# Kernel optimization log

Measured on AMD Instinct MI355X. Metric: run time of the kernel, lower is better.

The kernel has to match this reference:

```python
import jax, jax.numpy as jnp
import numpy as np

M, N, T = 4, 48, 512
D_IN = M + N                 # GRU-net input dim (m+n)
H1 = D_IN * 10 * 8           # 4160
HID = M * M + N * N          # 2320 GRU hidden
H2 = M * N * 4               # 768
D_OUT = M * N                # 192


def setup_inputs() -> dict:
    key = jax.random.key(0)
    ks = jax.random.split(key, 12)
    s = lambda i, shape, sc=0.02: (jax.random.normal(ks[i], shape, jnp.float32) * sc)
    return {
        "A": jnp.eye(M, dtype=jnp.float32) + s(0, (M, M), 0.05),
        "C": s(1, (N, M + 1), 0.1),
        "x0": jax.random.normal(ks[2], (M,), jnp.float32),
        "h0": jax.random.normal(ks[3], (HID,), jnp.float32),  # randn init hidden (zero_hidden_state=False)
        "y_seq": jax.random.normal(ks[4], (N, T), jnp.float32),
        "W1": s(5, (H1, D_IN)), "b1": jnp.zeros((H1,), jnp.float32),
        "W_ih": s(6, (3 * HID, H1)), "W_hh": s(7, (3 * HID, HID)),
        "b_ih": jnp.zeros((3 * HID,), jnp.float32), "b_hh": jnp.zeros((3 * HID,), jnp.float32),
        "W2": s(8, (H2, HID)), "b2": jnp.zeros((H2,), jnp.float32),
        "W3": s(9, (D_OUT, H2)), "b3": jnp.zeros((D_OUT,), jnp.float32),
    }


def _l2norm(v):
    # torch F.normalize(p=2, eps=1e-12): v / max(||v||, eps)
    return v / jnp.maximum(jnp.linalg.norm(v), 1e-12)


def _gru_cell(x, h, W_ih, W_hh, b_ih, b_hh):
    gi = W_ih @ x + b_ih
    gh = W_hh @ h + b_hh
    i_r, i_z, i_n = jnp.split(gi, 3)
    h_r, h_z, h_n = jnp.split(gh, 3)
    r = jax.nn.sigmoid(i_r + h_r)
    z = jax.nn.sigmoid(i_z + h_z)
    n = jnp.tanh(i_n + r * h_n)
    return (1.0 - z) * n + z * h


def reference(A, C, x0, h0, y_seq, W1, b1, W_ih, W_hh, b_ih, b_hh, W2, b2, W3, b3):
    one = jnp.ones((1,), jnp.float32)

    def step(carry, y):
        x_prior, x_post, h = carry
        # step_prior (linear case)
        x_prev_prior = x_prior
        x_prior = A @ x_post
        m1y = C @ jnp.concatenate([x_prior, one])  # [N]
        # step_KGain_est: KGainNet_in = [norm(dy), norm(dx)]
        knet_in = jnp.concatenate([_l2norm(y - m1y), _l2norm(x_post - x_prev_prior)])
        l1 = jax.nn.relu(W1 @ knet_in + b1)
        h = _gru_cell(l1, h, W_ih, W_hh, b_ih, b_hh)
        l2 = jax.nn.relu(W2 @ h + b2)
        kg = ((W3 @ l2 + b3) / 10000.0).reshape(M, N)
        # KNet_step posterior update
        x_post = x_prior + kg @ (y - m1y)
        return (x_prior, x_post, h), x_post

    _, xs = jax.lax.scan(step, (x0, x0, h0), y_seq.T)  # scan over T
    return xs.T  # [M, T], matches forward_sequence output
```

## Files before the change

kernel.cpp:

```cpp
#include <hip/hip_runtime.h>
#include <stdint.h>
#include <stddef.h>

typedef float v2f __attribute__((ext_vector_type(2)));

#define HID   2320
#define G3    6960
#define KIH   4160
#define KHH   2320
#define NBLK  232
#define NTHR  512
#define UPB   10
#define TSEQ  512
#define KRES  1600
#define INVWS (1.0f/128.0f)
#define SPINCAP (1u<<17)

#define WS_WIH8 0L
#define WS_W1E  28953600L
#define WS_HBP  29219840L
#define WS_SLT  29279232L
#define WS_END  29308928L

struct Offs {
  int l1s, hs, wih, whh, w2s, w3s, cs, as_, b3s, bih, bhh, b2s, gis, ghs,
      ts, inn, kn, dxs, xpri, xpo, b4, nrm, slp;
  int total;
};

__host__ __device__ inline Offs mkoffs(int res) {
  Offs o; int p = 0;
#define ALLOC(name, bytes) { p = (p + 15) & ~15; o.name = p; p += (bytes); }
  ALLOC(l1s, KIH*4) ALLOC(hs, HID*4)
  ALLOC(wih, res ? 30*KRES : 16) ALLOC(whh, res ? 30*KHH : 16)
  ALLOC(w2s, res ? 4*HID : 16)
  ALLOC(w3s, 16*48*4) ALLOC(cs, 240*4) ALLOC(as_, 64) ALLOC(b3s, 192*4)
  ALLOC(bih, 120) ALLOC(bhh, 120) ALLOC(b2s, 16)
  ALLOC(gis, 120) ALLOC(ghs, 120)
  ALLOC(ts, 64) ALLOC(inn, 192) ALLOC(kn, 256)
  ALLOC(dxs, 16) ALLOC(xpri, 16) ALLOC(xpo, 16) ALLOC(b4, 16) ALLOC(nrm, 16)
  ALLOC(slp, 64)
#undef ALLOC
  o.total = (p + 63) & ~63;
  return o;
}

struct Params {
  const float *A, *C, *x0, *h0, *y, *W1, *b1, *Wih, *Whh, *bih, *bhh, *W2, *b2, *W3, *b3;
  const uint8_t *wih8, *w1e;
  uint64_t *hbp, *slt;
  float *out;
  int resident;
};

__device__ __forceinline__ uint8_t f2fp8(float v) {
  v = fminf(fmaxf(v * 128.f, -448.f), 448.f);
  int pk = __builtin_amdgcn_cvt_pk_fp8_f32(v, v, 0, false);
  return (uint8_t)(pk & 0xff);
}

__device__ __forceinline__ void pub64(uint64_t* a, uint32_t tag, float v) {
  uint64_t w = ((uint64_t)tag << 32) | (uint64_t)__float_as_uint(v);
  __hip_atomic_store(a, w, __ATOMIC_RELAXED, __HIP_MEMORY_SCOPE_AGENT);
}

template<int N>
__device__ __forceinline__ void poll_pkt(const uint64_t* base, uint32_t want,
                                         float* out, bool& dead) {
  uint64_t v[N];
  uint32_t spins = 0;
  for (;;) {
    bool ok = true;
#pragma unroll
    for (int k = 0; k < N; ++k)
      v[k] = __hip_atomic_load(base + k, __ATOMIC_RELAXED, __HIP_MEMORY_SCOPE_AGENT);
#pragma unroll
    for (int k = 0; k < N; ++k) ok &= ((uint32_t)(v[k] >> 32) == want);
    if (ok || dead) break;
    __builtin_amdgcn_s_sleep(2);
    if (++spins > SPINCAP) dead = true;
  }
#pragma unroll
  for (int k = 0; k < N; ++k) out[k] = __uint_as_float((uint32_t)v[k]);
}

__device__ __forceinline__ void dot8_lds(
    const float* __restrict__ acts, const uint8_t* __restrict__ w, int stride,
    int K, const int* lrows, int nr, int lane, float acc[4])
{
  int kb = 0;
  for (; kb + 256 <= K; kb += 256) {
    const float4 a = ((const float4*)(acts + kb))[lane];
#pragma unroll
    for (int j = 0; j < 4; ++j) if (j < nr) {
      uint32_t wb = *(const uint32_t*)(w + (size_t)lrows[j]*stride + kb + (lane<<2));
      v2f lo = __builtin_amdgcn_cvt_pk_f32_fp8((int)wb, false);
      v2f hi = __builtin_amdgcn_cvt_pk_f32_fp8((int)wb, true);
      acc[j] = fmaf(lo.x, a.x, acc[j]); acc[j] = fmaf(lo.y, a.y, acc[j]);
      acc[j] = fmaf(hi.x, a.z, acc[j]); acc[j] = fmaf(hi.y, a.w, acc[j]);
    }
  }
  int rem = K - kb;
  if ((lane << 2) < rem) {
    const float4 a = ((const float4*)(acts + kb))[lane];
#pragma unroll
    for (int j = 0; j < 4; ++j) if (j < nr) {
      uint32_t wb = *(const uint32_t*)(w + (size_t)lrows[j]*stride + kb + (lane<<2));
      v2f lo = __builtin_amdgcn_cvt_pk_f32_fp8((int)wb, false);
      v2f hi = __builtin_amdgcn_cvt_pk_f32_fp8((int)wb, true);
      acc[j] = fmaf(lo.x, a.x, acc[j]); acc[j] = fmaf(lo.y, a.y, acc[j]);
      acc[j] = fmaf(hi.x, a.z, acc[j]); acc[j] = fmaf(hi.y, a.w, acc[j]);
    }
  }
}

__device__ __forceinline__ void dot8_glb(
    const float* __restrict__ acts, const uint8_t* __restrict__ gw, int gstride,
    int K0, int K, const int* grows, int nr, int lane, float acc[4])
{
  int kb = K0;
  for (; kb + 512 <= K; kb += 512) {
    const float4 a0 = ((const float4*)(acts + kb))[lane*2];
    const float4 a1 = ((const float4*)(acts + kb))[lane*2 + 1];
#pragma unroll
    for (int j = 0; j < 4; ++j) if (j < nr) {
      uint2 wb = *(const uint2*)(gw + (size_t)grows[j]*gstride + kb + (lane<<3));
      v2f l0 = __builtin_amdgcn_cvt_pk_f32_fp8((int)wb.x, false);
      v2f h0 = __builtin_amdgcn_cvt_pk_f32_fp8((int)wb.x, true);
      v2f l1 = __builtin_amdgcn_cvt_pk_f32_fp8((int)wb.y, false);
      v2f h1 = __builtin_amdgcn_cvt_pk_f32_fp8((int)wb.y, true);
      acc[j] = fmaf(l0.x, a0.x, acc[j]); acc[j] = fmaf(l0.y, a0.y, acc[j]);
      acc[j] = fmaf(h0.x, a0.z, acc[j]); acc[j] = fmaf(h0.y, a0.w, acc[j]);
      acc[j] = fmaf(l1.x, a1.x, acc[j]); acc[j] = fmaf(l1.y, a1.y, acc[j]);
      acc[j] = fmaf(h1.x, a1.z, acc[j]); acc[j] = fmaf(h1.y, a1.w, acc[j]);
    }
  }
  for (int e = kb + lane; e < K; e += 64) {
    float a = acts[e];
#pragma unroll
    for (int j = 0; j < 4; ++j) if (j < nr) {
      v2f lo = __builtin_amdgcn_cvt_pk_f32_fp8(
          (int)(uint32_t)gw[(size_t)grows[j]*gstride + e], false);
      acc[j] = fmaf(lo.x, a, acc[j]);
    }
  }
}

__device__ __forceinline__ void dotf_glb(
    const float* __restrict__ acts, const float* __restrict__ gw, int gstride,
    int K, const int* grows, int nr, int lane, float acc[4])
{
  for (int k = lane; k < K; k += 64) {
    float a = acts[k];
#pragma unroll
    for (int j = 0; j < 4; ++j) if (j < nr)
      acc[j] = fmaf(gw[(size_t)grows[j]*gstride + k], a, acc[j]);
  }
}

extern "C" __global__ void __launch_bounds__(NTHR, 2) knet_main(Params p)
{
  extern __shared__ char smem[];
  const Offs o = mkoffs(p.resident);
  float*   L1S  = (float*)(smem + o.l1s);
  float*   HS   = (float*)(smem + o.hs);
  uint8_t* WIHR = (uint8_t*)(smem + o.wih);
  uint8_t* WHHR = (uint8_t*)(smem + o.whh);
  uint8_t* W2S  = (uint8_t*)(smem + o.w2s);
  float*   W3S  = (float*)(smem + o.w3s);
  float*   CS   = (float*)(smem + o.cs);
  float*   AS   = (float*)(smem + o.as_);
  float*   B3S  = (float*)(smem + o.b3s);
  float*   BIH  = (float*)(smem + o.bih);
  float*   BHH  = (float*)(smem + o.bhh);
  float*   B2S  = (float*)(smem + o.b2s);
  float*   GIS  = (float*)(smem + o.gis);
  float*   GHS  = (float*)(smem + o.ghs);
  float*   TS   = (float*)(smem + o.ts);
  float*   INNS = (float*)(smem + o.inn);
  float*   KN   = (float*)(smem + o.kn);
  float*   DXS  = (float*)(smem + o.dxs);
  float*   XPRI = (float*)(smem + o.xpri);
  float*   XPO  = (float*)(smem + o.xpo);
  float*   B4   = (float*)(smem + o.b4);
  float*   NRM  = (float*)(smem + o.nrm);
  float*   SLP  = (float*)(smem + o.slp);

  const int tid  = (int)threadIdx.x;
  const int bid  = (int)blockIdx.x;
  const int lane = tid & 63;
  const int wv   = tid >> 6;
  const int rows2 = (bid < 72) ? 4 : 3;
  const int r2s   = (bid < 72) ? bid*4 : 288 + (bid-72)*3;
  bool dead = false;

  int lrows[4] = {0,0,0,0}, grows[4] = {0,0,0,0};
  int nr = 0;
#pragma unroll
  for (int j = 0; j < 4; ++j) {
    int row = wv + 8*j;
    if (row < 30) { int u = row/3, g = row - 3*u;
      lrows[nr] = row; grows[nr] = g*HID + bid*UPB + u; ++nr; }
  }

  for (int i = tid; i < rows2*192; i += NTHR) { int rl = i/192, rem = i - rl*192;
    W3S[i] = p.W3[(size_t)rem*768 + (r2s + rl)]; }
  for (int i = tid; i < 240; i += NTHR) CS[i] = p.C[i];
  if (tid < 16) AS[tid] = p.A[tid];
  for (int i = tid; i < 192; i += NTHR) B3S[i] = p.b3[i];
  if (tid < rows2) B2S[tid] = p.b2[r2s + tid];
  if (tid < 30) {
    int u = tid/3, g = tid - 3*u, ug = bid*UPB + u;
    BIH[tid] = p.bih[g*HID + ug];
    BHH[tid] = p.bhh[g*HID + ug];
  }
  for (int i = tid; i < HID; i += NTHR) HS[i] = p.h0[i];
  if (p.resident) {
    const int kd = KRES >> 2;
    uint32_t* W32 = (uint32_t*)WIHR;
    for (int i = tid; i < 30*kd; i += NTHR) {
      int row = i / kd, c = i - row*kd;
      int u = row/3, g = row - 3*u, gr = g*HID + bid*UPB + u;
      W32[i] = ((const uint32_t*)p.wih8)[(size_t)gr*(KIH/4) + c];
    }
    for (int i = tid; i < 30*KHH; i += NTHR) {
      int row = i / KHH, k = i - row*KHH;
      int u = row/3, g = row - 3*u, gr = g*HID + bid*UPB + u;
      WHHR[i] = f2fp8(p.Whh[(size_t)gr*KHH + k]);
    }
    for (int i = tid; i < rows2*HID; i += NTHR) {
      int rl = i / HID, k = i - rl*HID;
      W2S[i] = f2fp8(p.W2[(size_t)(r2s+rl)*HID + k]);
    }
  }
  uint2 pf[4][5];
#pragma unroll
  for (int j = 0; j < 4; ++j)
#pragma unroll
    for (int i = 0; i < 5; ++i) pf[j][i] = make_uint2(0u, 0u);
#pragma unroll
  for (int j = 0; j < 4; ++j) if (j < nr)
#pragma unroll
    for (int i = 0; i < 5; ++i)
      pf[j][i] = *(const uint2*)(p.wih8 + (size_t)grows[j]*KIH + KRES + i*512 + (lane<<3));
  __syncthreads();

  auto small_chain = [&](int ycol) {
    if (tid < 48) {
      float s = CS[tid*5 + 4];
#pragma unroll
      for (int k = 0; k < 4; ++k) s += CS[tid*5 + k] * XPRI[k];
      INNS[tid] = p.y[(size_t)tid*TSEQ + ycol] - s;
    }
    __syncthreads();
    if (tid == 0) {
      float s = 0;
      for (int j = 0; j < 48; ++j) s += INNS[j]*INNS[j];
      NRM[0] = fmaxf(sqrtf(s), 1e-12f);
      float s2 = 0;
      for (int j = 0; j < 4; ++j) s2 += DXS[j]*DXS[j];
      NRM[1] = fmaxf(sqrtf(s2), 1e-12f);
    }
    __syncthreads();
    if (tid < 48) KN[tid] = INNS[tid] / NRM[0];
    else if (tid < 52) KN[tid] = DXS[tid-48] / NRM[1];
    else if (tid == 52) KN[tid] = 1.0f;
    else if (tid < 64) KN[tid] = 0.0f;
    else if (tid < 68) {
      int i = tid - 64; float s = 0;
      for (int j = 0; j < 48; ++j) s += B3S[i*48 + j] * INNS[j];
      B4[i] = s;
    }
    if (tid >= 128 && tid < 128 + rows2*4) {
      int idx = tid - 128, rl = idx >> 2, i = idx & 3;
      float s = 0;
      for (int j = 0; j < 48; ++j) s += W3S[rl*192 + i*48 + j] * INNS[j];
      TS[i*4 + rl] = s;
    }
    __syncthreads();
    {
      float4 kn[16];
#pragma unroll
      for (int c = 0; c < 16; ++c) kn[c] = ((const float4*)KN)[c];
      for (int r = tid; r < KIH; r += NTHR) {
        const uint4* wp = (const uint4*)(p.w1e + (size_t)r*64);
        float acc = 0.f;
#pragma unroll
        for (int q = 0; q < 4; ++q) {
          uint4 w = wp[q];
          v2f l0 = __builtin_amdgcn_cvt_pk_f32_fp8((int)w.x, false);
          v2f h0 = __builtin_amdgcn_cvt_pk_f32_fp8((int)w.x, true);
          v2f l1 = __builtin_amdgcn_cvt_pk_f32_fp8((int)w.y, false);
          v2f h1 = __builtin_amdgcn_cvt_pk_f32_fp8((int)w.y, true);
          v2f l2 = __builtin_amdgcn_cvt_pk_f32_fp8((int)w.z, false);
          v2f h2 = __builtin_amdgcn_cvt_pk_f32_fp8((int)w.z, true);
          v2f l3 = __builtin_amdgcn_cvt_pk_f32_fp8((int)w.w, false);
          v2f h3 = __builtin_amdgcn_cvt_pk_f32_fp8((int)w.w, true);
          float4 a0 = kn[q*4+0], a1 = kn[q*4+1], a2 = kn[q*4+2], a3 = kn[q*4+3];
          acc = fmaf(l0.x,a0.x,acc); acc = fmaf(l0.y,a0.y,acc);
          acc = fmaf(h0.x,a0.z,acc); acc = fmaf(h0.y,a0.w,acc);
          acc = fmaf(l1.x,a1.x,acc); acc = fmaf(l1.y,a1.y,acc);
          acc = fmaf(h1.x,a1.z,acc); acc = fmaf(h1.y,a1.w,acc);
          acc = fmaf(l2.x,a2.x,acc); acc = fmaf(l2.y,a2.y,acc);
          acc = fmaf(h2.x,a2.z,acc); acc = fmaf(h2.y,a2.w,acc);
          acc = fmaf(l3.x,a3.x,acc); acc = fmaf(l3.y,a3.y,acc);
          acc = fmaf(h3.x,a3.z,acc); acc = fmaf(h3.y,a3.w,acc);
        }
        L1S[r] = fmaxf(acc * INVWS, 0.f);
      }
    }
    __syncthreads();
  };

  auto ghh = [&]() {
    float acc[4] = {0,0,0,0};
    if (p.resident) dot8_lds(HS, WHHR, KHH, KHH, lrows, nr, lane, acc);
    else            dotf_glb(HS, p.Whh, KHH, KHH, grows, nr, lane, acc);
#pragma unroll
    for (int m = 32; m >= 1; m >>= 1)
#pragma unroll
      for (int j = 0; j < 4; ++j) acc[j] += __shfl_xor(acc[j], m, 64);
    if (lane == 0)
#pragma unroll
      for (int j = 0; j < 4; ++j) if (j < nr) GHS[lrows[j]] = acc[j];
  };

  if (tid < 4) { XPO[tid] = p.x0[tid]; DXS[tid] = 0.f; }
  __syncthreads();
  if (tid < 4) {
    float s = 0;
#pragma unroll
    for (int j = 0; j < 4; ++j) s += AS[tid*4 + j] * XPO[j];
    XPRI[tid] = s;
  }
  __syncthreads();
  small_chain(0);
  ghh();
  __syncthreads();

  for (int t = 0; t < TSEQ; ++t) {
    const int par = t & 1;
    const uint32_t want = (uint32_t)(t + 1);

    {
      float acc[4] = {0,0,0,0};
      if (p.resident) dot8_lds(L1S, WIHR, KRES, KRES, lrows, nr, lane, acc);
      else            dot8_glb(L1S, p.wih8, KIH, 0, KRES, grows, nr, lane, acc);
#pragma unroll
      for (int i = 0; i < 5; ++i) {
        const float4 a0 = ((const float4*)(L1S + KRES + i*512))[lane*2];
        const float4 a1 = ((const float4*)(L1S + KRES + i*512))[lane*2 + 1];
#pragma unroll
        for (int j = 0; j < 4; ++j) if (j < nr) {
          uint2 w = pf[j][i];
          v2f l0 = __builtin_amdgcn_cvt_pk_f32_fp8((int)w.x, false);
          v2f h0 = __builtin_amdgcn_cvt_pk_f32_fp8((int)w.x, true);
          v2f l1v = __builtin_amdgcn_cvt_pk_f32_fp8((int)w.y, false);
          v2f h1 = __builtin_amdgcn_cvt_pk_f32_fp8((int)w.y, true);
          acc[j] = fmaf(l0.x, a0.x, acc[j]); acc[j] = fmaf(l0.y, a0.y, acc[j]);
          acc[j] = fmaf(h0.x, a0.z, acc[j]); acc[j] = fmaf(h0.y, a0.w, acc[j]);
          acc[j] = fmaf(l1v.x, a1.x, acc[j]); acc[j] = fmaf(l1v.y, a1.y, acc[j]);
          acc[j] = fmaf(h1.x, a1.z, acc[j]); acc[j] = fmaf(h1.y, a1.w, acc[j]);
        }
      }
#pragma unroll
      for (int m = 32; m >= 1; m >>= 1)
#pragma unroll
        for (int j = 0; j < 4; ++j) acc[j] += __shfl_xor(acc[j], m, 64);
      if (lane == 0)
#pragma unroll
        for (int j = 0; j < 4; ++j) if (j < nr) GIS[lrows[j]] = acc[j];
    }
    __syncthreads();

    if (tid < UPB) {
      int ug = bid*UPB + tid, r0 = tid*3;
      float gi0 = GIS[r0+0]*INVWS + BIH[r0+0], gh0 = GHS[r0+0]*INVWS + BHH[r0+0];
      float gi1 = GIS[r0+1]*INVWS + BIH[r0+1], gh1 = GHS[r0+1]*INVWS + BHH[r0+1];
      float gi2 = GIS[r0+2]*INVWS + BIH[r0+2], gh2 = GHS[r0+2]*INVWS + BHH[r0+2];
      float rg = 1.f/(1.f + expf(-(gi0+gh0)));
      float zg = 1.f/(1.f + expf(-(gi1+gh1)));
      float ng = tanhf(gi2 + rg*gh2);
      float hnew = (1.f - zg)*ng + zg*HS[ug];
      pub64(p.hbp + (((size_t)par*NBLK + bid) << 4) + tid, want, hnew);
    }
    __syncthreads();

    if (wv < 4) {
      int idx = (wv << 6) | lane;
      if (idx < NBLK) {
        float v[10];
        poll_pkt<10>(p.hbp + (((size_t)par*NBLK + idx) << 4), want, v, dead);
#pragma unroll
        for (int k = 0; k < 10; ++k) HS[idx*10 + k] = v[k];
      }
    }
    __syncthreads();

    if (wv == 0) {
      float a2[4] = {0,0,0,0};
      if (p.resident) {
        int kb = 0;
        for (; kb + 256 <= HID; kb += 256) {
          const float4 a = ((const float4*)(HS + kb))[lane];
#pragma unroll
          for (int rl = 0; rl < 4; ++rl) if (rl < rows2) {
            uint32_t wb = *(const uint32_t*)(W2S + rl*HID + kb + (lane<<2));
            v2f lo = __builtin_amdgcn_cvt_pk_f32_fp8((int)wb, false);
            v2f hi = __builtin_amdgcn_cvt_pk_f32_fp8((int)wb, true);
            a2[rl] = fmaf(lo.x, a.x, a2[rl]); a2[rl] = fmaf(lo.y, a.y, a2[rl]);
            a2[rl] = fmaf(hi.x, a.z, a2[rl]); a2[rl] = fmaf(hi.y, a.w, a2[rl]);
          }
        }
        if ((lane << 2) < HID - kb) {
          const float4 a = ((const float4*)(HS + kb))[lane];
#pragma unroll
          for (int rl = 0; rl < 4; ++rl) if (rl < rows2) {
            uint32_t wb = *(const uint32_t*)(W2S + rl*HID + kb + (lane<<2));
            v2f lo = __builtin_amdgcn_cvt_pk_f32_fp8((int)wb, false);
            v2f hi = __builtin_amdgcn_cvt_pk_f32_fp8((int)wb, true);
            a2[rl] = fmaf(lo.x, a.x, a2[rl]); a2[rl] = fmaf(lo.y, a.y, a2[rl]);
            a2[rl] = fmaf(hi.x, a.z, a2[rl]); a2[rl] = fmaf(hi.y, a.w, a2[rl]);
          }
        }
#pragma unroll
        for (int rl = 0; rl < 4; ++rl) a2[rl] *= INVWS;
      } else {
        for (int k = lane; k < HID; k += 64) {
          float a = HS[k];
#pragma unroll
          for (int rl = 0; rl < 4; ++rl) if (rl < rows2)
            a2[rl] = fmaf(p.W2[(size_t)(r2s+rl)*HID + k], a, a2[rl]);
        }
      }
#pragma unroll
      for (int m = 32; m >= 1; m >>= 1)
#pragma unroll
        for (int rl = 0; rl < 4; ++rl) a2[rl] += __shfl_xor(a2[rl], m, 64);
      if (lane < 4) {
        float l2v[4];
#pragma unroll
        for (int rl = 0; rl < 4; ++rl)
          l2v[rl] = (rl < rows2) ? fmaxf(a2[rl] + B2S[rl], 0.f) : 0.f;
        float cp = l2v[0]*TS[lane*4+0] + l2v[1]*TS[lane*4+1]
                 + l2v[2]*TS[lane*4+2] + l2v[3]*TS[lane*4+3];
        pub64(p.slt + (((size_t)par*NBLK + bid) << 3) + lane, want, cp);
      }
    }

    ghh();

    if (wv < 4) {
      int idx = (wv << 6) | lane;
      float s0 = 0, s1 = 0, s2 = 0, s3 = 0;
      if (idx < NBLK) {
        float v[4];
        poll_pkt<4>(p.slt + (((size_t)par*NBLK + idx) << 3), want, v, dead);
        s0 = v[0]; s1 = v[1]; s2 = v[2]; s3 = v[3];
      }
#pragma unroll
      for (int m = 32; m >= 1; m >>= 1) {
        s0 += __shfl_xor(s0, m, 64); s1 += __shfl_xor(s1, m, 64);
        s2 += __shfl_xor(s2, m, 64); s3 += __shfl_xor(s3, m, 64);
      }
      if (lane == 0) {
        SLP[wv*4+0] = s0; SLP[wv*4+1] = s1; SLP[wv*4+2] = s2; SLP[wv*4+3] = s3;
      }
    }
    __syncthreads();

    if (tid < 4) {
      float c = SLP[tid] + SLP[4 + tid] + SLP[8 + tid] + SLP[12 + tid];
      float xp = XPRI[tid] + (c + B4[tid]) * 1e-4f;
      XPO[tid] = xp;
      if (bid == 0) p.out[(size_t)tid*TSEQ + t] = xp;
    }
    __syncthreads();
    if (t + 1 < TSEQ) {
      if (tid < 4) {
        float xo = XPO[tid];
        DXS[tid] = xo - XPRI[tid];
        float s = 0;
#pragma unroll
        for (int j = 0; j < 4; ++j) s += AS[tid*4 + j] * XPO[j];
        XPRI[tid] = s;
      }
      __syncthreads();
      small_chain(t + 1);
    }
  }
}

extern "C" __global__ void knet_cvt_fp8(const float* __restrict__ src,
                                        uint8_t* __restrict__ dst, long n4) {
  long stride = (long)gridDim.x * blockDim.x;
  for (long i = (long)blockIdx.x*blockDim.x + threadIdx.x; i < n4; i += stride) {
    float4 v = ((const float4*)src)[i];
    float a0 = fminf(fmaxf(v.x * 128.f, -448.f), 448.f);
    float a1 = fminf(fmaxf(v.y * 128.f, -448.f), 448.f);
    float a2 = fminf(fmaxf(v.z * 128.f, -448.f), 448.f);
    float a3 = fminf(fmaxf(v.w * 128.f, -448.f), 448.f);
    int pk = __builtin_amdgcn_cvt_pk_fp8_f32(a0, a1, 0, false);
    pk = __builtin_amdgcn_cvt_pk_fp8_f32(a2, a3, pk, true);
    ((uint32_t*)dst)[i] = (uint32_t)pk;
  }
}

extern "C" __global__ void knet_build_w1e(const float* __restrict__ W1,
                                          const float* __restrict__ b1,
                                          uint8_t* __restrict__ dst) {
  int r = blockIdx.x * blockDim.x + threadIdx.x;
  if (r >= KIH) return;
  float v[64];
#pragma unroll 13
  for (int q = 0; q < 13; ++q) {
    float4 w = ((const float4*)(W1 + (size_t)r*52))[q];
    v[q*4+0] = w.x; v[q*4+1] = w.y; v[q*4+2] = w.z; v[q*4+3] = w.w;
  }
  v[52] = b1[r];
  for (int i = 53; i < 64; ++i) v[i] = 0.f;
  uint32_t out[16];
#pragma unroll 16
  for (int d = 0; d < 16; ++d) {
    float a0 = fminf(fmaxf(v[d*4+0] * 128.f, -448.f), 448.f);
    float a1 = fminf(fmaxf(v[d*4+1] * 128.f, -448.f), 448.f);
    float a2 = fminf(fmaxf(v[d*4+2] * 128.f, -448.f), 448.f);
    float a3 = fminf(fmaxf(v[d*4+3] * 128.f, -448.f), 448.f);
    int pk = __builtin_amdgcn_cvt_pk_fp8_f32(a0, a1, 0, false);
    pk = __builtin_amdgcn_cvt_pk_fp8_f32(a2, a3, pk, true);
    out[d] = (uint32_t)pk;
  }
  uint4* dp = (uint4*)(dst + (size_t)r*64);
#pragma unroll 4
  for (int q = 0; q < 4; ++q)
    dp[q] = make_uint4(out[q*4+0], out[q*4+1], out[q*4+2], out[q*4+3]);
}

extern "C" void kernel_launch(void* const* d_in, const int* in_sizes, int n_in,
                              void* d_out, int out_size, void* d_ws, size_t ws_size,
                              hipStream_t stream)
{
  if (ws_size < (size_t)WS_END) return;
  uint8_t* ws = (uint8_t*)d_ws;

  knet_cvt_fp8<<<2048, 256, 0, stream>>>((const float*)d_in[7], ws + WS_WIH8,
                                         (long)G3*KIH/4);
  knet_build_w1e<<<(KIH + 255)/256, 256, 0, stream>>>(
      (const float*)d_in[5], (const float*)d_in[6], ws + WS_W1E);

  int resident = 1;
  Offs o = mkoffs(resident);
  hipError_t e = hipFuncSetAttribute((const void*)knet_main,
                                     hipFuncAttributeMaxDynamicSharedMemorySize,
                                     o.total);
  if (e != hipSuccess) {
    resident = 0; o = mkoffs(resident);
    (void)hipFuncSetAttribute((const void*)knet_main,
                              hipFuncAttributeMaxDynamicSharedMemorySize, o.total);
  }

  Params p;
  p.A   = (const float*)d_in[0];  p.C   = (const float*)d_in[1];
  p.x0  = (const float*)d_in[2];  p.h0  = (const float*)d_in[3];
  p.y   = (const float*)d_in[4];
  p.W1  = (const float*)d_in[5];  p.b1  = (const float*)d_in[6];
  p.Wih = (const float*)d_in[7];  p.Whh = (const float*)d_in[8];
  p.bih = (const float*)d_in[9];  p.bhh = (const float*)d_in[10];
  p.W2  = (const float*)d_in[11]; p.b2  = (const float*)d_in[12];
  p.W3  = (const float*)d_in[13]; p.b3  = (const float*)d_in[14];
  p.wih8 = ws + WS_WIH8;
  p.w1e  = ws + WS_W1E;
  p.hbp  = (uint64_t*)(ws + WS_HBP);
  p.slt  = (uint64_t*)(ws + WS_SLT);
  p.out  = (float*)d_out;
  p.resident = resident;

  knet_main<<<NBLK, NTHR, (size_t)o.total, stream>>>(p);
}
```

Before: 8.799 ms.

## Split W2 rows across four waves and shrink L2 reducer set to 192 blocks

Each of 192 blocks now computes exactly four W2 rows, one per wave (waves 4-7), instead of one wave handling three or four rows across all 232 blocks. The cross-block poll of layer-2 partials drops from 232 to 192 packets (three waves). Poll loops spin briefly before sleeping, and the two norm reductions use wave shuffles instead of a serial thread-0 loop. This shortens the serial chain in each timestep, at the cost of an extra block barrier, an LDS round-trip, and 40 blocks that publish no layer-2 result.

```diff
diff --git a/kernel.cpp b/kernel.cpp
--- a/kernel.cpp
+++ b/kernel.cpp
@@ -9,6 +9,7 @@
 #define KIH   4160
 #define KHH   2320
 #define NBLK  232
+#define NL2B  192
 #define NTHR  512
 #define UPB   10
 #define TSEQ  512
@@ -24,7 +25,7 @@
 
 struct Offs {
   int l1s, hs, wih, whh, w2s, w3s, cs, as_, b3s, bih, bhh, b2s, gis, ghs,
-      ts, inn, kn, dxs, xpri, xpo, b4, nrm, slp;
+      ts, inn, kn, dxs, xpri, xpo, b4, nrm, l2r, slp;
   int total;
 };
 
@@ -39,7 +40,7 @@
   ALLOC(gis, 120) ALLOC(ghs, 120)
   ALLOC(ts, 64) ALLOC(inn, 192) ALLOC(kn, 256)
   ALLOC(dxs, 16) ALLOC(xpri, 16) ALLOC(xpo, 16) ALLOC(b4, 16) ALLOC(nrm, 16)
-  ALLOC(slp, 64)
+  ALLOC(l2r, 16) ALLOC(slp, 64)
 #undef ALLOC
   o.total = (p + 63) & ~63;
   return o;
@@ -77,8 +78,9 @@
 #pragma unroll
     for (int k = 0; k < N; ++k) ok &= ((uint32_t)(v[k] >> 32) == want);
     if (ok || dead) break;
-    __builtin_amdgcn_s_sleep(2);
-    if (++spins > SPINCAP) dead = true;
+    ++spins;
+    if (spins > 8) __builtin_amdgcn_s_sleep(2);
+    if (spins > SPINCAP) dead = true;
   }
 #pragma unroll
   for (int k = 0; k < N; ++k) out[k] = __uint_as_float((uint32_t)v[k]);
@@ -184,14 +186,15 @@
   float*   XPO  = (float*)(smem + o.xpo);
   float*   B4   = (float*)(smem + o.b4);
   float*   NRM  = (float*)(smem + o.nrm);
+  float*   L2R  = (float*)(smem + o.l2r);
   float*   SLP  = (float*)(smem + o.slp);
 
   const int tid  = (int)threadIdx.x;
   const int bid  = (int)blockIdx.x;
   const int lane = tid & 63;
   const int wv   = tid >> 6;
-  const int rows2 = (bid < 72) ? 4 : 3;
-  const int r2s   = (bid < 72) ? bid*4 : 288 + (bid-72)*3;
+  const int rows2 = (bid < NL2B) ? 4 : 0;
+  const int r2s   = bid * 4;
   bool dead = false;
 
   int lrows[4] = {0,0,0,0}, grows[4] = {0,0,0,0};
@@ -253,13 +256,16 @@
       INNS[tid] = p.y[(size_t)tid*TSEQ + ycol] - s;
     }
     __syncthreads();
-    if (tid == 0) {
-      float s = 0;
-      for (int j = 0; j < 48; ++j) s += INNS[j]*INNS[j];
-      NRM[0] = fmaxf(sqrtf(s), 1e-12f);
-      float s2 = 0;
-      for (int j = 0; j < 4; ++j) s2 += DXS[j]*DXS[j];
-      NRM[1] = fmaxf(sqrtf(s2), 1e-12f);
+    if (wv == 0) {
+      float q = (lane < 48) ? INNS[lane]*INNS[lane] : 0.f;
+#pragma unroll
+      for (int m = 32; m >= 1; m >>= 1) q += __shfl_xor(q, m, 64);
+      if (lane == 0) NRM[0] = fmaxf(sqrtf(q), 1e-12f);
+    } else if (wv == 1) {
+      float q = (lane < 4) ? DXS[lane]*DXS[lane] : 0.f;
+#pragma unroll
+      for (int m = 32; m >= 1; m >>= 1) q += __shfl_xor(q, m, 64);
+      if (lane == 0) NRM[1] = fmaxf(sqrtf(q), 1e-12f);
     }
     __syncthreads();
     if (tid < 48) KN[tid] = INNS[tid] / NRM[0];
@@ -397,67 +403,50 @@
     }
     __syncthreads();
 
-    if (wv == 0) {
-      float a2[4] = {0,0,0,0};
+    if (rows2 && wv >= 4) {
+      const int rl = wv - 4;
+      float a2 = 0.f;
       if (p.resident) {
         int kb = 0;
         for (; kb + 256 <= HID; kb += 256) {
           const float4 a = ((const float4*)(HS + kb))[lane];
-#pragma unroll
-          for (int rl = 0; rl < 4; ++rl) if (rl < rows2) {
-            uint32_t wb = *(const uint32_t*)(W2S + rl*HID + kb + (lane<<2));
-            v2f lo = __builtin_amdgcn_cvt_pk_f32_fp8((int)wb, false);
-            v2f hi = __builtin_amdgcn_cvt_pk_f32_fp8((int)wb, true);
-            a2[rl] = fmaf(lo.x, a.x, a2[rl]); a2[rl] = fmaf(lo.y, a.y, a2[rl]);
-            a2[rl] = fmaf(hi.x, a.z, a2[rl]); a2[rl] = fmaf(hi.y, a.w, a2[rl]);
-          }
+          uint32_t wb = *(const uint32_t*)(W2S + rl*HID + kb + (lane<<2));
+          v2f lo = __builtin_amdgcn_cvt_pk_f32_fp8((int)wb, false);
+          v2f hi = __builtin_amdgcn_cvt_pk_f32_fp8((int)wb, true);
+          a2 = fmaf(lo.x, a.x, a2); a2 = fmaf(lo.y, a.y, a2);
+          a2 = fmaf(hi.x, a.z, a2); a2 = fmaf(hi.y, a.w, a2);
         }
         if ((lane << 2) < HID - kb) {
           const float4 a = ((const float4*)(HS + kb))[lane];
-#pragma unroll
-          for (int rl = 0; rl < 4; ++rl) if (rl < rows2) {
-            uint32_t wb = *(const uint32_t*)(W2S + rl*HID + kb + (lane<<2));
-            v2f lo = __builtin_amdgcn_cvt_pk_f32_fp8((int)wb, false);
-            v2f hi = __builtin_amdgcn_cvt_pk_f32_fp8((int)wb, true);
-            a2[rl] = fmaf(lo.x, a.x, a2[rl]); a2[rl] = fmaf(lo.y, a.y, a2[rl]);
-            a2[rl] = fmaf(hi.x, a.z, a2[rl]); a2[rl] = fmaf(hi.y, a.w, a2[rl]);
-          }
+          uint32_t wb = *(const uint32_t*)(W2S + rl*HID + kb + (lane<<2));
+          v2f lo = __builtin_amdgcn_cvt_pk_f32_fp8((int)wb, false);
+          v2f hi = __builtin_amdgcn_cvt_pk_f32_fp8((int)wb, true);
+          a2 = fmaf(lo.x, a.x, a2); a2 = fmaf(lo.y, a.y, a2);
+          a2 = fmaf(hi.x, a.z, a2); a2 = fmaf(hi.y, a.w, a2);
         }
-#pragma unroll
-        for (int rl = 0; rl < 4; ++rl) a2[rl] *= INVWS;
+        a2 *= INVWS;
       } else {
-        for (int k = lane; k < HID; k += 64) {
-          float a = HS[k];
-#pragma unroll
-          for (int rl = 0; rl < 4; ++rl) if (rl < rows2)
-            a2[rl] = fmaf(p.W2[(size_t)(r2s+rl)*HID + k], a, a2[rl]);
-        }
-      }
-#pragma unroll
-      for (int m = 32; m >= 1; m >>= 1)
-#pragma unroll
-        for (int rl = 0; rl < 4; ++rl) a2[rl] += __shfl_xor(a2[rl], m, 64);
-      if (lane < 4) {
-        float l2v[4];
-#pragma unroll
-        for (int rl = 0; rl < 4; ++rl)
-          l2v[rl] = (rl < rows2) ? fmaxf(a2[rl] + B2S[rl], 0.f) : 0.f;
-        float cp = l2v[0]*TS[lane*4+0] + l2v[1]*TS[lane*4+1]
-                 + l2v[2]*TS[lane*4+2] + l2v[3]*TS[lane*4+3];
-        pub64(p.slt + (((size_t)par*NBLK + bid) << 3) + lane, want, cp);
-      }
+        for (int k = lane; k < HID; k += 64)
+          a2 = fmaf(p.W2[(size_t)(r2s+rl)*HID + k], HS[k], a2);
+      }
+#pragma unroll
+      for (int m = 32; m >= 1; m >>= 1) a2 += __shfl_xor(a2, m, 64);
+      if (lane == 0) L2R[rl] = fmaxf(a2 + B2S[rl], 0.f);
+    }
+    __syncthreads();
+    if (rows2 && tid < 4) {
+      float cp = L2R[0]*TS[tid*4+0] + L2R[1]*TS[tid*4+1]
+               + L2R[2]*TS[tid*4+2] + L2R[3]*TS[tid*4+3];
+      pub64(p.slt + (((size_t)par*NBLK + bid) << 3) + tid, want, cp);
     }
 
     ghh();
 
-    if (wv < 4) {
+    if (wv < 3) {
       int idx = (wv << 6) | lane;
-      float s0 = 0, s1 = 0, s2 = 0, s3 = 0;
-      if (idx < NBLK) {
-        float v[4];
-        poll_pkt<4>(p.slt + (((size_t)par*NBLK + idx) << 3), want, v, dead);
-        s0 = v[0]; s1 = v[1]; s2 = v[2]; s3 = v[3];
-      }
+      float v[4];
+      poll_pkt<4>(p.slt + (((size_t)par*NBLK + idx) << 3), want, v, dead);
+      float s0 = v[0], s1 = v[1], s2 = v[2], s3 = v[3];
 #pragma unroll
       for (int m = 32; m >= 1; m >>= 1) {
         s0 += __shfl_xor(s0, m, 64); s1 += __shfl_xor(s1, m, 64);
@@ -470,7 +459,7 @@
     __syncthreads();
 
     if (tid < 4) {
-      float c = SLP[tid] + SLP[4 + tid] + SLP[8 + tid] + SLP[12 + tid];
+      float c = SLP[tid] + SLP[4 + tid] + SLP[8 + tid];
       float xp = XPRI[tid] + (c + B4[tid]) * 1e-4f;
       XPO[tid] = xp;
       if (bid == 0) p.out[(size_t)tid*TSEQ + t] = xp;
```

After: 8.290 ms. -5.8%, faster.
